# Optimization experiments

Measured on AMD Instinct MI355X. Metric: run time of the kernel, lower is better.

Reference implementation:

```python
import jax, jax.numpy as jnp
import numpy as np
import math

DIM = 1024
NUM_HEADS = 16
HEAD_DIM = DIM // NUM_HEADS
MAX_SEQ_LEN = 2048


def setup_inputs() -> dict:
    key = jax.random.key(0)
    ks = jax.random.split(key, 10)
    B, S = 4, 2048
    std = 1.0 / math.sqrt(DIM)
    inp = {
        "x": jax.random.normal(ks[0], (B, S, DIM), dtype=jnp.float32),
        "key_padding_mask": jnp.zeros((B, S), dtype=jnp.bool_),
        "q_w": jax.random.uniform(ks[1], (DIM, DIM), minval=-std, maxval=std),
        "q_b": jax.random.uniform(ks[2], (DIM,), minval=-std, maxval=std),
        "k_w": jax.random.uniform(ks[3], (DIM, DIM), minval=-std, maxval=std),
        "k_b": jax.random.uniform(ks[4], (DIM,), minval=-std, maxval=std),
        "v_w": jax.random.uniform(ks[5], (DIM, DIM), minval=-std, maxval=std),
        "v_b": jax.random.uniform(ks[6], (DIM,), minval=-std, maxval=std),
        "o_w": jax.random.uniform(ks[7], (DIM, DIM), minval=-std, maxval=std),
        "o_b": jax.random.uniform(ks[8], (DIM,), minval=-std, maxval=std),
    }
    return inp


def _rope_tables(seq_len):
    # freqs over half the head dim, per the RotaryPositionalEmbedding module
    half = HEAD_DIM // 2
    freqs = 1.0 / (10000.0 ** (jnp.arange(0, HEAD_DIM, 2, dtype=jnp.float32) / HEAD_DIM))
    pos = jnp.arange(seq_len, dtype=jnp.float32)
    ang = jnp.outer(pos, freqs)  # [S, half]
    return jnp.cos(ang)[:, :half], jnp.sin(ang)[:, :half]


def _apply_rope(t, cos, sin):
    # t: [B, H, S, D]; rotate first/second halves (non-interleaved variant)
    half = HEAD_DIM // 2
    left, right = t[..., :half], t[..., half:]
    return jnp.concatenate([left * cos - right * sin,
                            left * sin + right * cos], axis=-1)


def reference(x, key_padding_mask, q_w, q_b, k_w, k_b, v_w, v_b, o_w, o_b):
    B, S, _ = x.shape
    scale = HEAD_DIM ** -0.5

    def proj(w, b):
        y = jnp.einsum('bsd,ed->bse', x, w) + b  # torch Linear: x @ W^T + b
        return y.reshape(B, S, NUM_HEADS, HEAD_DIM).transpose(0, 2, 1, 3)

    q = proj(q_w, q_b)  # [B, H, S, D]
    k = proj(k_w, k_b)
    v = proj(v_w, v_b)

    cos, sin = _rope_tables(S)  # [S, half], broadcast over B,H
    q = _apply_rope(q, cos, sin)
    k = _apply_rope(k, cos, sin)

    scores = jnp.einsum('bhqd,bhkd->bhqk', q, k) * scale
    scores = jnp.where(key_padding_mask[:, None, None, :], -1e9, scores)
    weights = jax.nn.softmax(scores, axis=-1)  # dropout p=0.0 -> identity
    out = jnp.einsum('bhqk,bhkd->bhqd', weights, v)
    out = out.transpose(0, 2, 1, 3).reshape(B, S, DIM)
    return jnp.einsum('bsd,ed->bse', out, o_w) + o_b
```

## Files before the change

kernel.cpp:

```cpp
#include <hip/hip_runtime.h>
#include <stdint.h>

#define SEQ   2048
#define BATCH 4
#define NH    16
#define HD    64
#define DIMN  1024
#define MROWS (BATCH*SEQ)

typedef __attribute__((ext_vector_type(8))) short          bf16x8;
typedef __attribute__((ext_vector_type(8))) unsigned short ushort8;
typedef __attribute__((ext_vector_type(4))) float          f32x4;

static __device__ __forceinline__ unsigned short f2bf(float f) {
    unsigned int u = __builtin_bit_cast(unsigned int, f);
    u += 0x7fffu + ((u >> 16) & 1u);
    return (unsigned short)(u >> 16);
}
static __device__ __forceinline__ unsigned int pack2bf(float lo, float hi) {
    unsigned int a = __builtin_bit_cast(unsigned int, lo) + 0x8000u;
    unsigned int b = __builtin_bit_cast(unsigned int, hi) + 0x8000u;
    return __builtin_amdgcn_perm(b, a, 0x07060302u);
}

__global__ __launch_bounds__(256) void cast_bf16_kernel(const float* __restrict__ src,
                                                        unsigned short* __restrict__ dst, int n) {
    int i = (blockIdx.x * 256 + threadIdx.x) * 8;
    if (i >= n) return;
    float4 a = *(const float4*)(src + i);
    float4 b = *(const float4*)(src + i + 4);
    ushort8 o;
    o[0]=f2bf(a.x); o[1]=f2bf(a.y); o[2]=f2bf(a.z); o[3]=f2bf(a.w);
    o[4]=f2bf(b.x); o[5]=f2bf(b.y); o[6]=f2bf(b.z); o[7]=f2bf(b.w);
    *(ushort8*)(dst + i) = o;
}

__global__ __launch_bounds__(256) void cast4_kernel(const float* __restrict__ s0, const float* __restrict__ s1,
                                                    const float* __restrict__ s2, const float* __restrict__ s3,
                                                    unsigned short* __restrict__ d0, unsigned short* __restrict__ d1,
                                                    unsigned short* __restrict__ d2, unsigned short* __restrict__ d3) {
    const float* s; unsigned short* d;
    switch (blockIdx.y) {
        case 0:  s = s0; d = d0; break;
        case 1:  s = s1; d = d1; break;
        case 2:  s = s2; d = d2; break;
        default: s = s3; d = d3; break;
    }
    int i = (blockIdx.x * 256 + threadIdx.x) * 8;
    float4 a = *(const float4*)(s + i);
    float4 b = *(const float4*)(s + i + 4);
    ushort8 o;
    o[0]=f2bf(a.x); o[1]=f2bf(a.y); o[2]=f2bf(a.z); o[3]=f2bf(a.w);
    o[4]=f2bf(b.x); o[5]=f2bf(b.y); o[6]=f2bf(b.z); o[7]=f2bf(b.w);
    *(ushort8*)(d + i) = o;
}

__global__ __launch_bounds__(256) void rope_tables_kernel(float* __restrict__ cosT,
                                                          float* __restrict__ sinT) {
    int idx = blockIdx.x * 256 + threadIdx.x;
    int s = idx >> 5, j = idx & 31;
    float t = (float)(2 * j) / 64.0f;
    float freq = 1.0f / powf(10000.0f, t);
    float ang  = (float)s * freq;
    cosT[idx] = cosf(ang);
    sinT[idx] = sinf(ang);
}

__global__ __launch_bounds__(128) void mask64_kernel(const unsigned char* __restrict__ mask,
                                                     unsigned long long* __restrict__ m64) {
    int t = threadIdx.x;
    int b = t >> 5, kt = t & 31;
    const unsigned char* p = mask + b * SEQ + kt * 64;
    unsigned long long v = 0;
    for (int j = 0; j < 64; j++) v |= (unsigned long long)(p[j] != 0) << j;
    m64[t] = v;
}

__global__ __launch_bounds__(256) void gemm_qk(const unsigned short* __restrict__ A,
        const unsigned short* __restrict__ Wq, const unsigned short* __restrict__ Wk,
        const float* __restrict__ bq, const float* __restrict__ bk,
        unsigned short* __restrict__ Qo, unsigned short* __restrict__ Ko,
        const float* __restrict__ cosT, const float* __restrict__ sinT) {
    __shared__ __align__(16) unsigned short As[128 * 32];
    __shared__ __align__(16) unsigned short Bs[128 * 32];
    const int which = blockIdx.x >> 3;
    const int n0    = (blockIdx.x & 7) * 128;
    const unsigned short* W = which == 0 ? Wq : Wk;
    const float* bias       = which == 0 ? bq : bk;
    unsigned short* Out     = which == 0 ? Qo : Ko;
    const float scale = which == 0 ? 0.18033688011112042f : 1.0f;
    const int tid  = threadIdx.x;
    const int wid  = tid >> 6, lane = tid & 63;
    const int quad = lane >> 4, l15 = lane & 15;
    const int wm   = wid >> 1,  wn  = wid & 1;
    const int m0   = blockIdx.y * 128;

    f32x4 acc[4][4];
#pragma unroll
    for (int i = 0; i < 4; i++)
#pragma unroll
        for (int j = 0; j < 4; j++) acc[i][j] = (f32x4)0.0f;

    const int rb = wid * 32 + (lane >> 2);
    const int cb = (lane & 3) * 8;

    for (int k0 = 0; k0 < DIMN; k0 += 32) {
#pragma unroll
        for (int i = 0; i < 2; i++) {
            const unsigned short* ga = A + (size_t)(m0 + rb + i * 16) * DIMN + k0 + cb;
            __builtin_amdgcn_global_load_lds((const __attribute__((address_space(1))) void*)ga,
                (__attribute__((address_space(3))) void*)&As[(wid * 32 + i * 16) * 32], 16, 0, 0);
            const unsigned short* gb = W + (size_t)(n0 + rb + i * 16) * DIMN + k0 + cb;
            __builtin_amdgcn_global_load_lds((const __attribute__((address_space(1))) void*)gb,
                (__attribute__((address_space(3))) void*)&Bs[(wid * 32 + i * 16) * 32], 16, 0, 0);
        }
        __syncthreads();
        bf16x8 af[4], bfr[4];
#pragma unroll
        for (int f = 0; f < 4; f++) af[f]  = *(const bf16x8*)&As[(wm * 64 + f * 16 + l15) * 32 + quad * 8];
#pragma unroll
        for (int f = 0; f < 4; f++) bfr[f] = *(const bf16x8*)&Bs[(wn * 64 + f * 16 + l15) * 32 + quad * 8];
#pragma unroll
        for (int fm = 0; fm < 4; fm++)
#pragma unroll
            for (int fn = 0; fn < 4; fn++)
                acc[fm][fn] = __builtin_amdgcn_mfma_f32_16x16x32_bf16(af[fm], bfr[fn], acc[fm][fn], 0, 0, 0);
        __syncthreads();
    }

    float bv4[4];
#pragma unroll
    for (int fn = 0; fn < 4; fn++) bv4[fn] = bias[n0 + wn * 64 + fn * 16 + l15];
    const int h = (n0 >> 6) + wn;

#pragma unroll
    for (int fm = 0; fm < 4; fm++)
#pragma unroll
        for (int r = 0; r < 4; r++) {
            int mrow = m0 + wm * 64 + fm * 16 + quad * 4 + r;
            int b = mrow >> 11, s = mrow & (SEQ - 1);
            unsigned short* orow = Out + ((size_t)(b * NH + h) * SEQ + s) * HD;
            float v0 = (acc[fm][0][r] + bv4[0]) * scale;
            float v1 = (acc[fm][1][r] + bv4[1]) * scale;
            float v2 = (acc[fm][2][r] + bv4[2]) * scale;
            float v3 = (acc[fm][3][r] + bv4[3]) * scale;
            int d0 = l15, d1 = 16 + l15;
            float c0 = cosT[s * 32 + d0], s0 = sinT[s * 32 + d0];
            float c1 = cosT[s * 32 + d1], s1 = sinT[s * 32 + d1];
            orow[d0]      = f2bf(v0 * c0 - v2 * s0);
            orow[d0 + 32] = f2bf(v0 * s0 + v2 * c0);
            orow[d1]      = f2bf(v1 * c1 - v3 * s1);
            orow[d1 + 32] = f2bf(v1 * s1 + v3 * c1);
        }
}

__global__ __launch_bounds__(256) void gemm_vt(const unsigned short* __restrict__ Wv,
                                               const unsigned short* __restrict__ X,
                                               const float* __restrict__ bias,
                                               unsigned short* __restrict__ Vt) {
    __shared__ __align__(16) unsigned short As[128 * 32];
    __shared__ __align__(16) unsigned short Bs[128 * 32];
    const int tid  = threadIdx.x;
    const int wid  = tid >> 6, lane = tid & 63;
    const int quad = lane >> 4, l15 = lane & 15;
    const int wm   = wid >> 1,  wn  = wid & 1;
    const int m0   = blockIdx.y * 128;
    const int n0   = blockIdx.x * 128;

    f32x4 acc[4][4];
#pragma unroll
    for (int i = 0; i < 4; i++)
#pragma unroll
        for (int j = 0; j < 4; j++) acc[i][j] = (f32x4)0.0f;

    const int rb = wid * 32 + (lane >> 2);
    const int cb = (lane & 3) * 8;

    for (int k0 = 0; k0 < DIMN; k0 += 32) {
#pragma unroll
        for (int i = 0; i < 2; i++) {
            const unsigned short* ga = Wv + (size_t)(m0 + rb + i * 16) * DIMN + k0 + cb;
            __builtin_amdgcn_global_load_lds((const __attribute__((address_space(1))) void*)ga,
                (__attribute__((address_space(3))) void*)&As[(wid * 32 + i * 16) * 32], 16, 0, 0);
            const unsigned short* gb = X + (size_t)(n0 + rb + i * 16) * DIMN + k0 + cb;
            __builtin_amdgcn_global_load_lds((const __attribute__((address_space(1))) void*)gb,
                (__attribute__((address_space(3))) void*)&Bs[(wid * 32 + i * 16) * 32], 16, 0, 0);
        }
        __syncthreads();
        bf16x8 af[4], bfr[4];
#pragma unroll
        for (int f = 0; f < 4; f++) af[f]  = *(const bf16x8*)&As[(wm * 64 + f * 16 + l15) * 32 + quad * 8];
#pragma unroll
        for (int f = 0; f < 4; f++) bfr[f] = *(const bf16x8*)&Bs[(wn * 64 + f * 16 + l15) * 32 + quad * 8];
#pragma unroll
        for (int fm = 0; fm < 4; fm++)
#pragma unroll
            for (int fn = 0; fn < 4; fn++)
                acc[fm][fn] = __builtin_amdgcn_mfma_f32_16x16x32_bf16(af[fm], bfr[fn], acc[fm][fn], 0, 0, 0);
        __syncthreads();
    }

    float4 bb[4];
#pragma unroll
    for (int fm = 0; fm < 4; fm++)
        bb[fm] = *(const float4*)&bias[m0 + wm * 64 + fm * 16 + quad * 4];

    const int b     = n0 >> 11;
    const int sbase = (n0 & (SEQ - 1)) + wn * 64 + l15;
#pragma unroll
    for (int fm = 0; fm < 4; fm++)
#pragma unroll
        for (int r = 0; r < 4; r++) {
            int e = m0 + wm * 64 + fm * 16 + quad * 4 + r;
            float bval = r == 0 ? bb[fm].x : (r == 1 ? bb[fm].y : (r == 2 ? bb[fm].z : bb[fm].w));
            unsigned short* row = Vt + ((size_t)(b * NH + (e >> 6)) * HD + (e & 63)) * SEQ + sbase;
#pragma unroll
            for (int fn = 0; fn < 4; fn++)
                row[fn * 16] = f2bf(acc[fm][fn][r] + bval);
        }
}

__global__ __launch_bounds__(256) void gemm_bt(const unsigned short* __restrict__ A,
                                               const unsigned short* __restrict__ W,
                                               const float* __restrict__ bias,
                                               float* __restrict__ out) {
    __shared__ __align__(16) unsigned short As[128 * 32];
    __shared__ __align__(16) unsigned short Bs[128 * 32];
    const int tid  = threadIdx.x;
    const int wid  = tid >> 6, lane = tid & 63;
    const int quad = lane >> 4, l15 = lane & 15;
    const int wm   = wid >> 1,  wn  = wid & 1;
    const int m0   = blockIdx.y * 128, n0 = blockIdx.x * 128;

    f32x4 acc[4][4];
#pragma unroll
    for (int i = 0; i < 4; i++)
#pragma unroll
        for (int j = 0; j < 4; j++) acc[i][j] = (f32x4)0.0f;

    const int rb = wid * 32 + (lane >> 2);
    const int cb = (lane & 3) * 8;

    for (int k0 = 0; k0 < DIMN; k0 += 32) {
#pragma unroll
        for (int i = 0; i < 2; i++) {
            const unsigned short* ga = A + (size_t)(m0 + rb + i * 16) * DIMN + k0 + cb;
            __builtin_amdgcn_global_load_lds((const __attribute__((address_space(1))) void*)ga,
                (__attribute__((address_space(3))) void*)&As[(wid * 32 + i * 16) * 32], 16, 0, 0);
            const unsigned short* gb = W + (size_t)(n0 + rb + i * 16) * DIMN + k0 + cb;
            __builtin_amdgcn_global_load_lds((const __attribute__((address_space(1))) void*)gb,
                (__attribute__((address_space(3))) void*)&Bs[(wid * 32 + i * 16) * 32], 16, 0, 0);
        }
        __syncthreads();
        bf16x8 af[4], bfr[4];
#pragma unroll
        for (int f = 0; f < 4; f++) af[f]  = *(const bf16x8*)&As[(wm * 64 + f * 16 + l15) * 32 + quad * 8];
#pragma unroll
        for (int f = 0; f < 4; f++) bfr[f] = *(const bf16x8*)&Bs[(wn * 64 + f * 16 + l15) * 32 + quad * 8];
#pragma unroll
        for (int fm = 0; fm < 4; fm++)
#pragma unroll
            for (int fn = 0; fn < 4; fn++)
                acc[fm][fn] = __builtin_amdgcn_mfma_f32_16x16x32_bf16(af[fm], bfr[fn], acc[fm][fn], 0, 0, 0);
        __syncthreads();
    }

    float bv4[4];
#pragma unroll
    for (int fn = 0; fn < 4; fn++) bv4[fn] = bias[n0 + wn * 64 + fn * 16 + l15];
#pragma unroll
    for (int fm = 0; fm < 4; fm++)
#pragma unroll
        for (int r = 0; r < 4; r++) {
            int mrow = m0 + wm * 64 + fm * 16 + quad * 4 + r;
            float* orow = out + (size_t)mrow * DIMN + n0 + wn * 64;
#pragma unroll
            for (int fn = 0; fn < 4; fn++) orow[fn * 16 + l15] = acc[fm][fn][r] + bv4[fn];
        }
}

__global__ __launch_bounds__(256, 4) void attn_kernel(const unsigned short* __restrict__ Q,
                                                      const unsigned short* __restrict__ K,
                                                      const unsigned short* __restrict__ Vt,
                                                      const unsigned long long* __restrict__ M64,
                                                      unsigned short* __restrict__ Ob) {
    __shared__ __align__(16) unsigned short Ks[64 * 72];
    __shared__ __align__(16) unsigned short Vs[64 * 72];
    __shared__ __align__(16) unsigned short Ps[4 * 32 * 72];

    const int tid  = threadIdx.x;
    const int wid  = tid >> 6, lane = tid & 63;
    const int quad = lane >> 4, l15 = lane & 15;
    const int bh = blockIdx.y, b = bh >> 4, h = bh & 15;
    const int q0 = blockIdx.x * 128;

    bf16x8 qf[2][2];
#pragma unroll
    for (int n = 0; n < 2; n++) {
        const int qs = q0 + wid * 32 + n * 16 + l15;
#pragma unroll
        for (int ks = 0; ks < 2; ks++)
            qf[n][ks] = __builtin_bit_cast(bf16x8,
                *(const uint4*)&Q[((size_t)bh * SEQ + qs) * HD + ks * 32 + quad * 8]);
    }

    f32x4 Oa[4][2];
#pragma unroll
    for (int i = 0; i < 4; i++)
#pragma unroll
        for (int n = 0; n < 2; n++) Oa[i][n] = (f32x4)0.0f;
    float ls[2] = {0.0f, 0.0f};

    unsigned short* Pw = &Ps[wid * 32 * 72];
    const int sr = tid >> 2;
    const int sc = (tid & 3) * 8;
    const unsigned short* Kg = K + (size_t)bh * SEQ * HD;
    const unsigned short* Vg = Vt + ((size_t)bh * HD + sr) * SEQ + sc;

    for (int kt = 0; kt < SEQ / 64; kt++) {
        const int k0 = kt * 64;
        uint4 ka[2], va[2];
#pragma unroll
        for (int i = 0; i < 2; i++) ka[i] = *(const uint4*)&Kg[(size_t)(k0 + sr) * HD + sc + i * 32];
#pragma unroll
        for (int i = 0; i < 2; i++) va[i] = *(const uint4*)&Vg[k0 + i * 32];
        unsigned long long mb = M64[b * (SEQ / 64) + kt];
#pragma unroll
        for (int i = 0; i < 2; i++) *(uint4*)&Ks[sr * 72 + sc + i * 32] = ka[i];
#pragma unroll
        for (int i = 0; i < 2; i++) *(uint4*)&Vs[sr * 72 + sc + i * 32] = va[i];
        __syncthreads();

        f32x4 st[4][2];
#pragma unroll
        for (int f = 0; f < 4; f++) {
            bf16x8 kf0 = *(const bf16x8*)&Ks[(f * 16 + l15) * 72 + quad * 8];
            bf16x8 kf1 = *(const bf16x8*)&Ks[(f * 16 + l15) * 72 + 32 + quad * 8];
#pragma unroll
            for (int n = 0; n < 2; n++) {
                st[f][n] = __builtin_amdgcn_mfma_f32_16x16x32_bf16(kf0, qf[n][0], (f32x4)0.0f, 0, 0, 0);
                st[f][n] = __builtin_amdgcn_mfma_f32_16x16x32_bf16(kf1, qf[n][1], st[f][n], 0, 0, 0);
            }
        }

        if (mb) {
#pragma unroll
            for (int f = 0; f < 4; f++)
#pragma unroll
                for (int n = 0; n < 2; n++)
#pragma unroll
                    for (int r = 0; r < 4; r++) {
                        int kk = f * 16 + quad * 4 + r;
                        if ((mb >> kk) & 1ull) st[f][n][r] = -1e9f;
                    }
        }

#pragma unroll
        for (int f = 0; f < 4; f++)
#pragma unroll
            for (int n = 0; n < 2; n++) {
                float p0 = exp2f(st[f][n][0]);
                float p1 = exp2f(st[f][n][1]);
                float p2 = exp2f(st[f][n][2]);
                float p3 = exp2f(st[f][n][3]);
                ls[n] += (p0 + p1) + (p2 + p3);
                uint2 w;
                w.x = pack2bf(p0, p1);
                w.y = pack2bf(p2, p3);
                *(uint2*)&Pw[(n * 16 + l15) * 72 + f * 16 + quad * 4] = w;
            }

#pragma unroll
        for (int ks = 0; ks < 2; ks++) {
            bf16x8 pf[2];
#pragma unroll
            for (int n = 0; n < 2; n++)
                pf[n] = *(const bf16x8*)&Pw[(n * 16 + l15) * 72 + ks * 32 + quad * 8];
#pragma unroll
            for (int df = 0; df < 4; df++) {
                bf16x8 vf = *(const bf16x8*)&Vs[(df * 16 + l15) * 72 + ks * 32 + quad * 8];
#pragma unroll
                for (int n = 0; n < 2; n++)
                    Oa[df][n] = __builtin_amdgcn_mfma_f32_16x16x32_bf16(vf, pf[n], Oa[df][n], 0, 0, 0);
            }
        }
        __syncthreads();
    }

    float linv[2];
#pragma unroll
    for (int n = 0; n < 2; n++) {
        float l = ls[n];
        l += __shfl_xor(l, 16);
        l += __shfl_xor(l, 32);
        linv[n] = 1.0f / l;
    }

#pragma unroll
    for (int n = 0; n < 2; n++) {
        int s = q0 + wid * 32 + n * 16 + l15;
        unsigned short* orow = Ob + ((size_t)b * SEQ + s) * DIMN + h * HD + quad * 4;
#pragma unroll
        for (int df = 0; df < 4; df++) {
            uint2 w;
            w.x = pack2bf(Oa[df][n][0] * linv[n], Oa[df][n][1] * linv[n]);
            w.y = pack2bf(Oa[df][n][2] * linv[n], Oa[df][n][3] * linv[n]);
            *(uint2*)&orow[df * 16] = w;
        }
    }
}

extern "C" void kernel_launch(void* const* d_in, const int* in_sizes, int n_in,
                              void* d_out, int out_size, void* d_ws, size_t ws_size,
                              hipStream_t stream) {
    (void)in_sizes; (void)n_in; (void)out_size; (void)ws_size;
    const float* x  = (const float*)d_in[0];
    const unsigned char* mask = (const unsigned char*)d_in[1];
    const float* q_w = (const float*)d_in[2];
    const float* q_b = (const float*)d_in[3];
    const float* k_w = (const float*)d_in[4];
    const float* k_b = (const float*)d_in[5];
    const float* v_w = (const float*)d_in[6];
    const float* v_b = (const float*)d_in[7];
    const float* o_w = (const float*)d_in[8];
    const float* o_b = (const float*)d_in[9];
    float* out = (float*)d_out;

    char* w = (char*)d_ws;
    unsigned short* xb = (unsigned short*)w;
    unsigned short* wq = (unsigned short*)(w + (16u << 20));
    unsigned short* wk = wq + (1u << 20);
    unsigned short* wv = wk + (1u << 20);
    unsigned short* wo = wv + (1u << 20);
    float* cosT = (float*)(w + (24u << 20));
    float* sinT = cosT + SEQ * 32;
    unsigned long long* m64 = (unsigned long long*)(w + (24u << 20) + (1u << 19));
    unsigned short* Qb  = (unsigned short*)(w + (25u << 20));
    unsigned short* Kb  = Qb + (8u << 20);
    unsigned short* Vtb = Kb + (8u << 20);
    unsigned short* Ob  = xb;

    cast_bf16_kernel<<<dim3(MROWS * DIMN / 2048), 256, 0, stream>>>(x, xb, MROWS * DIMN);
    cast4_kernel<<<dim3(DIMN * DIMN / 2048, 4), 256, 0, stream>>>(q_w, k_w, v_w, o_w, wq, wk, wv, wo);
    rope_tables_kernel<<<dim3(SEQ * 32 / 256), 256, 0, stream>>>(cosT, sinT);
    mask64_kernel<<<dim3(1), 128, 0, stream>>>(mask, m64);

    gemm_qk<<<dim3(16, 64), 256, 0, stream>>>(xb, wq, wk, q_b, k_b, Qb, Kb, cosT, sinT);
    gemm_vt<<<dim3(64, 8), 256, 0, stream>>>(wv, xb, v_b, Vtb);

    attn_kernel<<<dim3(SEQ / 128, BATCH * NH), 256, 0, stream>>>(Qb, Kb, Vtb, m64, Ob);

    gemm_bt<<<dim3(DIMN / 128, MROWS / 128), 256, 0, stream>>>(Ob, wo, o_b, out);
}
```

Before: 341.3 us.

## Merge QK and V projections into one launch; enlarge attention query tile with K/V prefetch

The Q/K and transposed-V projection GEMMs are merged into a single launch whose grid covers all three outputs, removing one launch and filling the GPU better. The attention kernel now processes 256 queries per block (64 per wave), which doubles K/V reuse per LDS load. It register-prefetches the next K/V tile and mask word while computing the current one, and splits each 64-key tile into two 32-key halves to shrink the P staging buffer. P is packed to bf16 by truncation instead of rounding, which is cheaper but slightly less accurate. The cost is higher register pressure (launch bound lowered to 3 blocks) and half as many attention blocks.

```diff
diff --git a/kernel.cpp b/kernel.cpp
--- a/kernel.cpp
+++ b/kernel.cpp
@@ -21,6 +21,10 @@
     unsigned int a = __builtin_bit_cast(unsigned int, lo) + 0x8000u;
     unsigned int b = __builtin_bit_cast(unsigned int, hi) + 0x8000u;
     return __builtin_amdgcn_perm(b, a, 0x07060302u);
+}
+static __device__ __forceinline__ unsigned int pack2bf_trunc(float lo, float hi) {
+    return __builtin_amdgcn_perm(__builtin_bit_cast(unsigned int, hi),
+                                 __builtin_bit_cast(unsigned int, lo), 0x07060302u);
 }
 
 __global__ __launch_bounds__(256) void cast_bf16_kernel(const float* __restrict__ src,
@@ -76,24 +80,31 @@
     m64[t] = v;
 }
 
-__global__ __launch_bounds__(256) void gemm_qk(const unsigned short* __restrict__ A,
+__global__ __launch_bounds__(256) void gemm_qkvt(const unsigned short* __restrict__ X,
         const unsigned short* __restrict__ Wq, const unsigned short* __restrict__ Wk,
-        const float* __restrict__ bq, const float* __restrict__ bk,
-        unsigned short* __restrict__ Qo, unsigned short* __restrict__ Ko,
+        const unsigned short* __restrict__ Wv,
+        const float* __restrict__ bq, const float* __restrict__ bk, const float* __restrict__ bv,
+        unsigned short* __restrict__ Qo, unsigned short* __restrict__ Ko, unsigned short* __restrict__ Vto,
         const float* __restrict__ cosT, const float* __restrict__ sinT) {
     __shared__ __align__(16) unsigned short As[128 * 32];
     __shared__ __align__(16) unsigned short Bs[128 * 32];
     const int which = blockIdx.x >> 3;
-    const int n0    = (blockIdx.x & 7) * 128;
-    const unsigned short* W = which == 0 ? Wq : Wk;
-    const float* bias       = which == 0 ? bq : bk;
-    unsigned short* Out     = which == 0 ? Qo : Ko;
-    const float scale = which == 0 ? 0.18033688011112042f : 1.0f;
     const int tid  = threadIdx.x;
     const int wid  = tid >> 6, lane = tid & 63;
     const int quad = lane >> 4, l15 = lane & 15;
     const int wm   = wid >> 1,  wn  = wid & 1;
-    const int m0   = blockIdx.y * 128;
+
+    const unsigned short *Ag, *Bg;
+    int m0, n0;
+    if (which < 2) {
+        m0 = blockIdx.y * 128;
+        n0 = (blockIdx.x & 7) * 128;
+        Ag = X;  Bg = which == 0 ? Wq : Wk;
+    } else {
+        m0 = (blockIdx.x & 7) * 128;
+        n0 = blockIdx.y * 128;
+        Ag = Wv; Bg = X;
+    }
 
     f32x4 acc[4][4];
 #pragma unroll
@@ -107,10 +118,10 @@
     for (int k0 = 0; k0 < DIMN; k0 += 32) {
 #pragma unroll
         for (int i = 0; i < 2; i++) {
-            const unsigned short* ga = A + (size_t)(m0 + rb + i * 16) * DIMN + k0 + cb;
+            const unsigned short* ga = Ag + (size_t)(m0 + rb + i * 16) * DIMN + k0 + cb;
             __builtin_amdgcn_global_load_lds((const __attribute__((address_space(1))) void*)ga,
                 (__attribute__((address_space(3))) void*)&As[(wid * 32 + i * 16) * 32], 16, 0, 0);
-            const unsigned short* gb = W + (size_t)(n0 + rb + i * 16) * DIMN + k0 + cb;
+            const unsigned short* gb = Bg + (size_t)(n0 + rb + i * 16) * DIMN + k0 + cb;
             __builtin_amdgcn_global_load_lds((const __attribute__((address_space(1))) void*)gb,
                 (__attribute__((address_space(3))) void*)&Bs[(wid * 32 + i * 16) * 32], 16, 0, 0);
         }
@@ -128,96 +139,52 @@
         __syncthreads();
     }
 
-    float bv4[4];
-#pragma unroll
-    for (int fn = 0; fn < 4; fn++) bv4[fn] = bias[n0 + wn * 64 + fn * 16 + l15];
-    const int h = (n0 >> 6) + wn;
-
-#pragma unroll
-    for (int fm = 0; fm < 4; fm++)
-#pragma unroll
-        for (int r = 0; r < 4; r++) {
-            int mrow = m0 + wm * 64 + fm * 16 + quad * 4 + r;
-            int b = mrow >> 11, s = mrow & (SEQ - 1);
-            unsigned short* orow = Out + ((size_t)(b * NH + h) * SEQ + s) * HD;
-            float v0 = (acc[fm][0][r] + bv4[0]) * scale;
-            float v1 = (acc[fm][1][r] + bv4[1]) * scale;
-            float v2 = (acc[fm][2][r] + bv4[2]) * scale;
-            float v3 = (acc[fm][3][r] + bv4[3]) * scale;
-            int d0 = l15, d1 = 16 + l15;
-            float c0 = cosT[s * 32 + d0], s0 = sinT[s * 32 + d0];
-            float c1 = cosT[s * 32 + d1], s1 = sinT[s * 32 + d1];
-            orow[d0]      = f2bf(v0 * c0 - v2 * s0);
-            orow[d0 + 32] = f2bf(v0 * s0 + v2 * c0);
-            orow[d1]      = f2bf(v1 * c1 - v3 * s1);
-            orow[d1 + 32] = f2bf(v1 * s1 + v3 * c1);
-        }
-}
-
-__global__ __launch_bounds__(256) void gemm_vt(const unsigned short* __restrict__ Wv,
-                                               const unsigned short* __restrict__ X,
-                                               const float* __restrict__ bias,
-                                               unsigned short* __restrict__ Vt) {
-    __shared__ __align__(16) unsigned short As[128 * 32];
-    __shared__ __align__(16) unsigned short Bs[128 * 32];
-    const int tid  = threadIdx.x;
-    const int wid  = tid >> 6, lane = tid & 63;
-    const int quad = lane >> 4, l15 = lane & 15;
-    const int wm   = wid >> 1,  wn  = wid & 1;
-    const int m0   = blockIdx.y * 128;
-    const int n0   = blockIdx.x * 128;
-
-    f32x4 acc[4][4];
-#pragma unroll
-    for (int i = 0; i < 4; i++)
-#pragma unroll
-        for (int j = 0; j < 4; j++) acc[i][j] = (f32x4)0.0f;
-
-    const int rb = wid * 32 + (lane >> 2);
-    const int cb = (lane & 3) * 8;
-
-    for (int k0 = 0; k0 < DIMN; k0 += 32) {
-#pragma unroll
-        for (int i = 0; i < 2; i++) {
-            const unsigned short* ga = Wv + (size_t)(m0 + rb + i * 16) * DIMN + k0 + cb;
-            __builtin_amdgcn_global_load_lds((const __attribute__((address_space(1))) void*)ga,
-                (__attribute__((address_space(3))) void*)&As[(wid * 32 + i * 16) * 32], 16, 0, 0);
-            const unsigned short* gb = X + (size_t)(n0 + rb + i * 16) * DIMN + k0 + cb;
-            __builtin_amdgcn_global_load_lds((const __attribute__((address_space(1))) void*)gb,
-                (__attribute__((address_space(3))) void*)&Bs[(wid * 32 + i * 16) * 32], 16, 0, 0);
-        }
-        __syncthreads();
-        bf16x8 af[4], bfr[4];
-#pragma unroll
-        for (int f = 0; f < 4; f++) af[f]  = *(const bf16x8*)&As[(wm * 64 + f * 16 + l15) * 32 + quad * 8];
-#pragma unroll
-        for (int f = 0; f < 4; f++) bfr[f] = *(const bf16x8*)&Bs[(wn * 64 + f * 16 + l15) * 32 + quad * 8];
+    if (which < 2) {
+        const float* bias   = which == 0 ? bq : bk;
+        unsigned short* Out = which == 0 ? Qo : Ko;
+        const float scale = which == 0 ? 0.18033688011112042f : 1.0f;
+        float bv4[4];
+#pragma unroll
+        for (int fn = 0; fn < 4; fn++) bv4[fn] = bias[n0 + wn * 64 + fn * 16 + l15];
+        const int h = (n0 >> 6) + wn;
 #pragma unroll
         for (int fm = 0; fm < 4; fm++)
 #pragma unroll
-            for (int fn = 0; fn < 4; fn++)
-                acc[fm][fn] = __builtin_amdgcn_mfma_f32_16x16x32_bf16(af[fm], bfr[fn], acc[fm][fn], 0, 0, 0);
-        __syncthreads();
-    }
-
-    float4 bb[4];
-#pragma unroll
-    for (int fm = 0; fm < 4; fm++)
-        bb[fm] = *(const float4*)&bias[m0 + wm * 64 + fm * 16 + quad * 4];
-
-    const int b     = n0 >> 11;
-    const int sbase = (n0 & (SEQ - 1)) + wn * 64 + l15;
-#pragma unroll
-    for (int fm = 0; fm < 4; fm++)
-#pragma unroll
-        for (int r = 0; r < 4; r++) {
-            int e = m0 + wm * 64 + fm * 16 + quad * 4 + r;
-            float bval = r == 0 ? bb[fm].x : (r == 1 ? bb[fm].y : (r == 2 ? bb[fm].z : bb[fm].w));
-            unsigned short* row = Vt + ((size_t)(b * NH + (e >> 6)) * HD + (e & 63)) * SEQ + sbase;
-#pragma unroll
-            for (int fn = 0; fn < 4; fn++)
-                row[fn * 16] = f2bf(acc[fm][fn][r] + bval);
-        }
+            for (int r = 0; r < 4; r++) {
+                int mrow = m0 + wm * 64 + fm * 16 + quad * 4 + r;
+                int b = mrow >> 11, s = mrow & (SEQ - 1);
+                unsigned short* orow = Out + ((size_t)(b * NH + h) * SEQ + s) * HD;
+                float v0 = (acc[fm][0][r] + bv4[0]) * scale;
+                float v1 = (acc[fm][1][r] + bv4[1]) * scale;
+                float v2 = (acc[fm][2][r] + bv4[2]) * scale;
+                float v3 = (acc[fm][3][r] + bv4[3]) * scale;
+                int d0 = l15, d1 = 16 + l15;
+                float c0 = cosT[s * 32 + d0], s0 = sinT[s * 32 + d0];
+                float c1 = cosT[s * 32 + d1], s1 = sinT[s * 32 + d1];
+                orow[d0]      = f2bf(v0 * c0 - v2 * s0);
+                orow[d0 + 32] = f2bf(v0 * s0 + v2 * c0);
+                orow[d1]      = f2bf(v1 * c1 - v3 * s1);
+                orow[d1 + 32] = f2bf(v1 * s1 + v3 * c1);
+            }
+    } else {
+        float4 bb[4];
+#pragma unroll
+        for (int fm = 0; fm < 4; fm++)
+            bb[fm] = *(const float4*)&bv[m0 + wm * 64 + fm * 16 + quad * 4];
+        const int b     = n0 >> 11;
+        const int sbase = (n0 & (SEQ - 1)) + wn * 64 + l15;
+#pragma unroll
+        for (int fm = 0; fm < 4; fm++)
+#pragma unroll
+            for (int r = 0; r < 4; r++) {
+                int e = m0 + wm * 64 + fm * 16 + quad * 4 + r;
+                float bval = r == 0 ? bb[fm].x : (r == 1 ? bb[fm].y : (r == 2 ? bb[fm].z : bb[fm].w));
+                unsigned short* row = Vto + ((size_t)(b * NH + (e >> 6)) * HD + (e & 63)) * SEQ + sbase;
+#pragma unroll
+                for (int fn = 0; fn < 4; fn++)
+                    row[fn * 16] = f2bf(acc[fm][fn][r] + bval);
+            }
+    }
 }
 
 __global__ __launch_bounds__(256) void gemm_bt(const unsigned short* __restrict__ A,
@@ -279,117 +246,127 @@
         }
 }
 
-__global__ __launch_bounds__(256, 4) void attn_kernel(const unsigned short* __restrict__ Q,
+__global__ __launch_bounds__(256, 3) void attn_kernel(const unsigned short* __restrict__ Q,
                                                       const unsigned short* __restrict__ K,
                                                       const unsigned short* __restrict__ Vt,
                                                       const unsigned long long* __restrict__ M64,
                                                       unsigned short* __restrict__ Ob) {
     __shared__ __align__(16) unsigned short Ks[64 * 72];
     __shared__ __align__(16) unsigned short Vs[64 * 72];
-    __shared__ __align__(16) unsigned short Ps[4 * 32 * 72];
+    __shared__ __align__(16) unsigned short Ps[4 * 64 * 40];
 
     const int tid  = threadIdx.x;
     const int wid  = tid >> 6, lane = tid & 63;
     const int quad = lane >> 4, l15 = lane & 15;
     const int bh = blockIdx.y, b = bh >> 4, h = bh & 15;
-    const int q0 = blockIdx.x * 128;
-
-    bf16x8 qf[2][2];
-#pragma unroll
-    for (int n = 0; n < 2; n++) {
-        const int qs = q0 + wid * 32 + n * 16 + l15;
-#pragma unroll
-        for (int ks = 0; ks < 2; ks++)
-            qf[n][ks] = __builtin_bit_cast(bf16x8,
-                *(const uint4*)&Q[((size_t)bh * SEQ + qs) * HD + ks * 32 + quad * 8]);
-    }
-
-    f32x4 Oa[4][2];
+    const int q0 = blockIdx.x * 256;
+
+    bf16x8 qf[4][2];
+#pragma unroll
+    for (int n = 0; n < 4; n++) {
+        const int qs = q0 + wid * 64 + n * 16 + l15;
+#pragma unroll
+        for (int dk = 0; dk < 2; dk++)
+            qf[n][dk] = __builtin_bit_cast(bf16x8,
+                *(const uint4*)&Q[((size_t)bh * SEQ + qs) * HD + dk * 32 + quad * 8]);
+    }
+
+    f32x4 Oa[4][4];
 #pragma unroll
     for (int i = 0; i < 4; i++)
 #pragma unroll
-        for (int n = 0; n < 2; n++) Oa[i][n] = (f32x4)0.0f;
-    float ls[2] = {0.0f, 0.0f};
-
-    unsigned short* Pw = &Ps[wid * 32 * 72];
+        for (int n = 0; n < 4; n++) Oa[i][n] = (f32x4)0.0f;
+    float ls[4] = {0.0f, 0.0f, 0.0f, 0.0f};
+
+    unsigned short* Pw = &Ps[wid * 64 * 40];
     const int sr = tid >> 2;
     const int sc = (tid & 3) * 8;
     const unsigned short* Kg = K + (size_t)bh * SEQ * HD;
     const unsigned short* Vg = Vt + ((size_t)bh * HD + sr) * SEQ + sc;
 
+    uint4 ka[2], va[2];
+    unsigned long long mb;
+#pragma unroll
+    for (int i = 0; i < 2; i++) ka[i] = *(const uint4*)&Kg[(size_t)sr * HD + sc + i * 32];
+#pragma unroll
+    for (int i = 0; i < 2; i++) va[i] = *(const uint4*)&Vg[i * 32];
+    mb = M64[b * (SEQ / 64)];
+
     for (int kt = 0; kt < SEQ / 64; kt++) {
-        const int k0 = kt * 64;
-        uint4 ka[2], va[2];
-#pragma unroll
-        for (int i = 0; i < 2; i++) ka[i] = *(const uint4*)&Kg[(size_t)(k0 + sr) * HD + sc + i * 32];
-#pragma unroll
-        for (int i = 0; i < 2; i++) va[i] = *(const uint4*)&Vg[k0 + i * 32];
-        unsigned long long mb = M64[b * (SEQ / 64) + kt];
 #pragma unroll
         for (int i = 0; i < 2; i++) *(uint4*)&Ks[sr * 72 + sc + i * 32] = ka[i];
 #pragma unroll
         for (int i = 0; i < 2; i++) *(uint4*)&Vs[sr * 72 + sc + i * 32] = va[i];
-        __syncthreads();
-
-        f32x4 st[4][2];
-#pragma unroll
-        for (int f = 0; f < 4; f++) {
-            bf16x8 kf0 = *(const bf16x8*)&Ks[(f * 16 + l15) * 72 + quad * 8];
-            bf16x8 kf1 = *(const bf16x8*)&Ks[(f * 16 + l15) * 72 + 32 + quad * 8];
-#pragma unroll
-            for (int n = 0; n < 2; n++) {
-                st[f][n] = __builtin_amdgcn_mfma_f32_16x16x32_bf16(kf0, qf[n][0], (f32x4)0.0f, 0, 0, 0);
-                st[f][n] = __builtin_amdgcn_mfma_f32_16x16x32_bf16(kf1, qf[n][1], st[f][n], 0, 0, 0);
+        unsigned long long mbc = mb;
+        __syncthreads();
+
+        if (kt + 1 < SEQ / 64) {
+            const int k1 = (kt + 1) * 64;
+#pragma unroll
+            for (int i = 0; i < 2; i++) ka[i] = *(const uint4*)&Kg[(size_t)(k1 + sr) * HD + sc + i * 32];
+#pragma unroll
+            for (int i = 0; i < 2; i++) va[i] = *(const uint4*)&Vg[k1 + i * 32];
+            mb = M64[b * (SEQ / 64) + kt + 1];
+        }
+
+#pragma unroll
+        for (int h2 = 0; h2 < 2; h2++) {
+            f32x4 st[2][4];
+#pragma unroll
+            for (int f2 = 0; f2 < 2; f2++) {
+                const int f = h2 * 2 + f2;
+                bf16x8 kf0 = *(const bf16x8*)&Ks[(f * 16 + l15) * 72 + quad * 8];
+                bf16x8 kf1 = *(const bf16x8*)&Ks[(f * 16 + l15) * 72 + 32 + quad * 8];
+#pragma unroll
+                for (int n = 0; n < 4; n++) {
+                    st[f2][n] = __builtin_amdgcn_mfma_f32_16x16x32_bf16(kf0, qf[n][0], (f32x4)0.0f, 0, 0, 0);
+                    st[f2][n] = __builtin_amdgcn_mfma_f32_16x16x32_bf16(kf1, qf[n][1], st[f2][n], 0, 0, 0);
+                }
             }
-        }
-
-        if (mb) {
-#pragma unroll
-            for (int f = 0; f < 4; f++)
-#pragma unroll
-                for (int n = 0; n < 2; n++)
-#pragma unroll
-                    for (int r = 0; r < 4; r++) {
-                        int kk = f * 16 + quad * 4 + r;
-                        if ((mb >> kk) & 1ull) st[f][n][r] = -1e9f;
-                    }
-        }
-
-#pragma unroll
-        for (int f = 0; f < 4; f++)
-#pragma unroll
-            for (int n = 0; n < 2; n++) {
-                float p0 = exp2f(st[f][n][0]);
-                float p1 = exp2f(st[f][n][1]);
-                float p2 = exp2f(st[f][n][2]);
-                float p3 = exp2f(st[f][n][3]);
-                ls[n] += (p0 + p1) + (p2 + p3);
-                uint2 w;
-                w.x = pack2bf(p0, p1);
-                w.y = pack2bf(p2, p3);
-                *(uint2*)&Pw[(n * 16 + l15) * 72 + f * 16 + quad * 4] = w;
+            unsigned int mh = (unsigned int)(mbc >> (h2 * 32));
+            if (mh) {
+#pragma unroll
+                for (int f2 = 0; f2 < 2; f2++)
+#pragma unroll
+                    for (int n = 0; n < 4; n++)
+#pragma unroll
+                        for (int r = 0; r < 4; r++) {
+                            int kk = f2 * 16 + quad * 4 + r;
+                            if ((mh >> kk) & 1u) st[f2][n][r] = -1e9f;
+                        }
             }
-
-#pragma unroll
-        for (int ks = 0; ks < 2; ks++) {
-            bf16x8 pf[2];
-#pragma unroll
-            for (int n = 0; n < 2; n++)
-                pf[n] = *(const bf16x8*)&Pw[(n * 16 + l15) * 72 + ks * 32 + quad * 8];
+#pragma unroll
+            for (int f2 = 0; f2 < 2; f2++)
+#pragma unroll
+                for (int n = 0; n < 4; n++) {
+                    float p0 = exp2f(st[f2][n][0]);
+                    float p1 = exp2f(st[f2][n][1]);
+                    float p2 = exp2f(st[f2][n][2]);
+                    float p3 = exp2f(st[f2][n][3]);
+                    ls[n] += (p0 + p1) + (p2 + p3);
+                    uint2 w;
+                    w.x = pack2bf_trunc(p0, p1);
+                    w.y = pack2bf_trunc(p2, p3);
+                    *(uint2*)&Pw[(n * 16 + l15) * 40 + f2 * 16 + quad * 4] = w;
+                }
+            bf16x8 pf[4];
+#pragma unroll
+            for (int n = 0; n < 4; n++)
+                pf[n] = *(const bf16x8*)&Pw[(n * 16 + l15) * 40 + quad * 8];
 #pragma unroll
             for (int df = 0; df < 4; df++) {
-                bf16x8 vf = *(const bf16x8*)&Vs[(df * 16 + l15) * 72 + ks * 32 + quad * 8];
-#pragma unroll
-                for (int n = 0; n < 2; n++)
+                bf16x8 vf = *(const bf16x8*)&Vs[(df * 16 + l15) * 72 + h2 * 32 + quad * 8];
+#pragma unroll
+                for (int n = 0; n < 4; n++)
                     Oa[df][n] = __builtin_amdgcn_mfma_f32_16x16x32_bf16(vf, pf[n], Oa[df][n], 0, 0, 0);
             }
         }
         __syncthreads();
     }
 
-    float linv[2];
-#pragma unroll
-    for (int n = 0; n < 2; n++) {
+    float linv[4];
+#pragma unroll
+    for (int n = 0; n < 4; n++) {
         float l = ls[n];
         l += __shfl_xor(l, 16);
         l += __shfl_xor(l, 32);
@@ -397,8 +374,8 @@
     }
 
 #pragma unroll
-    for (int n = 0; n < 2; n++) {
-        int s = q0 + wid * 32 + n * 16 + l15;
+    for (int n = 0; n < 4; n++) {
+        int s = q0 + wid * 64 + n * 16 + l15;
         unsigned short* orow = Ob + ((size_t)b * SEQ + s) * DIMN + h * HD + quad * 4;
 #pragma unroll
         for (int df = 0; df < 4; df++) {
@@ -445,10 +422,10 @@
     rope_tables_kernel<<<dim3(SEQ * 32 / 256), 256, 0, stream>>>(cosT, sinT);
     mask64_kernel<<<dim3(1), 128, 0, stream>>>(mask, m64);
 
-    gemm_qk<<<dim3(16, 64), 256, 0, stream>>>(xb, wq, wk, q_b, k_b, Qb, Kb, cosT, sinT);
-    gemm_vt<<<dim3(64, 8), 256, 0, stream>>>(wv, xb, v_b, Vtb);
-
-    attn_kernel<<<dim3(SEQ / 128, BATCH * NH), 256, 0, stream>>>(Qb, Kb, Vtb, m64, Ob);
+    gemm_qkvt<<<dim3(24, 64), 256, 0, stream>>>(xb, wq, wk, wv, q_b, k_b, v_b,
+                                                Qb, Kb, Vtb, cosT, sinT);
+
+    attn_kernel<<<dim3(SEQ / 256, BATCH * NH), 256, 0, stream>>>(Qb, Kb, Vtb, m64, Ob);
 
     gemm_bt<<<dim3(DIMN / 128, MROWS / 128), 256, 0, stream>>>(Ob, wo, o_b, out);
 }
```

Measured after the change: 467.7 us. +37.0%, slower.
